# Kernel optimization log

Measured on AMD Instinct MI355X. Metric: run time of the kernel, lower is better.

## Reference

```python
import jax, jax.numpy as jnp
import numpy as np

N_NODES = 50000
N_GRAPHS = 256
IN_DIM = 128
HID = 128
N_LAYERS = 3
N_EDGES = 800000


def setup_inputs() -> dict:
    key = jax.random.key(0)
    ks = jax.random.split(key, 16)
    x = jax.random.normal(ks[0], (N_NODES, IN_DIM), dtype=jnp.float32)
    edge_index = jax.random.randint(ks[1], (2, N_EDGES), 0, N_NODES, dtype=jnp.int64)
    batch = jnp.sort(jax.random.randint(ks[2], (N_NODES,), 0, N_GRAPHS, dtype=jnp.int64))
    inp = {"x": x, "edge_index": edge_index, "batch": batch}
    # SAGEConv params per PyG: lin_l (bias) applied to mean-aggregated neighbors,
    # lin_r (no bias) applied to the root node feature.
    dims = [(IN_DIM, HID)] + [(HID, HID)] * (N_LAYERS - 1)
    for i, (din, dout) in enumerate(dims):
        s = 1.0 / np.sqrt(din)
        inp[f"Wl{i}"] = jax.random.uniform(ks[3 + 3 * i], (din, dout), jnp.float32, -s, s)
        inp[f"bl{i}"] = jax.random.uniform(ks[4 + 3 * i], (dout,), jnp.float32, -s, s)
        inp[f"Wr{i}"] = jax.random.uniform(ks[5 + 3 * i], (din, dout), jnp.float32, -s, s)
    return inp


def _sage_conv(x, src, dst, Wl, bl, Wr):
    # mean aggregation of source-node messages into destination nodes
    msg = x[src]                                               # [E, d] gather
    agg = jax.ops.segment_sum(msg, dst, num_segments=N_NODES)  # [N, d] scatter-add
    deg = jax.ops.segment_sum(jnp.ones((src.shape[0], 1), x.dtype), dst,
                              num_segments=N_NODES)
    agg = agg / jnp.maximum(deg, 1.0)
    return agg @ Wl + bl + x @ Wr


def reference(x, edge_index, batch, Wl0, bl0, Wr0, Wl1, bl1, Wr1, Wl2, bl2, Wr2):
    src, dst = edge_index[0], edge_index[1]
    params = [(Wl0, bl0, Wr0), (Wl1, bl1, Wr1), (Wl2, bl2, Wr2)]
    h = x
    for Wl, bl, Wr in params:
        h = jax.nn.relu(_sage_conv(h, src, dst, Wl, bl, Wr))
        # dropout is a no-op in eval mode
    # meanmax readout over graph ids
    cnt = jax.ops.segment_sum(jnp.ones((h.shape[0], 1), h.dtype), batch,
                              num_segments=N_GRAPHS)
    g_mean = jax.ops.segment_sum(h, batch, num_segments=N_GRAPHS) / jnp.maximum(cnt, 1.0)
    g_max = jax.ops.segment_max(h, batch, num_segments=N_GRAPHS)
    g_max = jnp.where(jnp.isfinite(g_max), g_max, 0.0)  # empty graphs -> 0
    return jnp.concatenate([g_mean, g_max], axis=-1)    # [G, 2*HID]
```

## Files before the change

kernel.cpp:

```cpp
#include <hip/hip_runtime.h>
#include <hip/hip_bf16.h>
#include <stdint.h>

#define N_NODES  50000
#define N_GRAPHS 256
#define DIM      128
#define N_EDGES  800000
#define K2       256
#define N_STRIPS (N_NODES / 16)
#define PAD_CAP  64
#define RO_ROWS  32

typedef __attribute__((ext_vector_type(8))) short  short8;
typedef __attribute__((ext_vector_type(4))) float  floatx4;
typedef __attribute__((ext_vector_type(4))) int    intx4;

__device__ __forceinline__ ushort f2bf(float f) {
    union { float f; uint32_t u; } c; c.f = f;
    uint32_t u = c.u;
    return (ushort)((u + 0x7fffu + ((u >> 16) & 1u)) >> 16);
}
__device__ __forceinline__ float bf2f(ushort b) {
    union { uint32_t u; float f; } c; c.u = ((uint32_t)b) << 16;
    return c.f;
}

#define MB_CONV 6250
#define MB_PREPW (MB_CONV + 384)
#define MB_GB   (MB_PREPW + 196)
#define MB_CNT  (MB_GB + 196)
#define MB_OUT  (MB_CNT + 256)
__global__ __launch_bounds__(256) void k_misc(const float* __restrict__ x, ushort* __restrict__ xb,
                                              const float* __restrict__ Wl0, const float* __restrict__ Wr0,
                                              const float* __restrict__ Wl1, const float* __restrict__ Wr1,
                                              const float* __restrict__ Wl2, const float* __restrict__ Wr2,
                                              ushort* __restrict__ Wt,
                                              const int* __restrict__ batch,
                                              int* __restrict__ gstart, int* __restrict__ gend,
                                              int* __restrict__ cnt, float* __restrict__ out) {
    int b = blockIdx.x, t = threadIdx.x;
    if (b < MB_CONV) {
        int i = b * 256 + t;
        float4 v = ((const float4*)x)[i];
        uint32_t lo = (uint32_t)f2bf(v.x) | ((uint32_t)f2bf(v.y) << 16);
        uint32_t hi = (uint32_t)f2bf(v.z) | ((uint32_t)f2bf(v.w) << 16);
        ((uint2*)xb)[i] = make_uint2(lo, hi);
    } else if (b < MB_PREPW) {
        int i = (b - MB_CONV) * 256 + t;
        int layer = i / (DIM * K2);
        int j = i % (DIM * K2);
        int n = j / K2, k = j % K2;
        const float* Wl = (layer == 0) ? Wl0 : (layer == 1) ? Wl1 : Wl2;
        const float* Wr = (layer == 0) ? Wr0 : (layer == 1) ? Wr1 : Wr2;
        float v = (k < DIM) ? Wl[k * DIM + n] : Wr[(k - DIM) * DIM + n];
        Wt[i] = f2bf(v);
    } else if (b < MB_GB) {
        int i = (b - MB_PREPW) * 256 + t;
        if (i < N_NODES) {
            int g = batch[i];
            if (i == 0) gstart[g] = 0;
            int gn = (i + 1 < N_NODES) ? batch[i + 1] : -1;
            if (gn != g) {
                gend[g] = i + 1;
                if (gn >= 0) gstart[gn] = i + 1;
            }
        }
    } else if (b < MB_CNT) {
        int i = (b - MB_GB) * 256 + t;
        if (i < N_NODES) cnt[i] = 0;
    } else {
        int i = (b - MB_CNT) * 256 + t;
        if (i < N_GRAPHS * 2 * DIM) out[i] = 0.f;
    }
}

__global__ __launch_bounds__(256) void k_build_direct(const int* __restrict__ src,
                                                      const int* __restrict__ dst,
                                                      int* __restrict__ cnt,
                                                      int* __restrict__ padded) {
    int i = blockIdx.x * 256 + threadIdx.x;
    if (i < N_EDGES) {
        int d = dst[i], s = src[i];
        int p = atomicAdd(&cnt[d], 1);
        if (p < PAD_CAP) padded[(size_t)d * PAD_CAP + p] = s;
    }
}

__global__ __launch_bounds__(256) void k_sort_adj(int* __restrict__ padded,
                                                  const int* __restrict__ cnt) {
    int wid  = threadIdx.x >> 6;
    int lane = threadIdx.x & 63;
    int node = blockIdx.x * 4 + wid;
    if (node >= N_NODES) return;
    int deg = cnt[node];
    int m   = deg < PAD_CAP ? deg : PAD_CAP;
    int* lst = padded + (size_t)node * PAD_CAP;
    int v = (lane < m) ? lst[lane] : 0x7fffffff;
    #pragma unroll
    for (int k = 2; k <= 64; k <<= 1) {
        #pragma unroll
        for (int j = k >> 1; j > 0; j >>= 1) {
            int other  = __shfl_xor(v, j, 64);
            bool down  = (lane & k) != 0;
            bool lower = (lane & j) == 0;
            v = (lower ^ down) ? min(v, other) : max(v, other);
        }
    }
    if (lane < m) lst[lane] = v;
}

template <bool OUT_F32>
__global__ __launch_bounds__(256) void k_layer(const ushort* __restrict__ h_in,
                                               const int* __restrict__ padded,
                                               const int* __restrict__ cnt,
                                               const ushort* __restrict__ Wt,
                                               const float* __restrict__ bias,
                                               ushort* __restrict__ out_bf,
                                               float* __restrict__ out_f) {
    __shared__ ushort sAgg[16 * DIM];
    __shared__ int    sIdx[16 * PAD_CAP];
    __shared__ int    sCnt[16];
    __shared__ int    sChl[4][17];
    __shared__ int    sNch[4];

    int t    = threadIdx.x;
    int wid  = t >> 6;
    int lane = t & 63;
    int r0   = blockIdx.x * 16;
    const uint32_t* hw = (const uint32_t*)h_in;

    ((intx4*)sIdx)[t] = __builtin_nontemporal_load(
        ((const intx4*)(padded + (size_t)r0 * PAD_CAP)) + t);
    if (t < 16) sCnt[t] = cnt[r0 + t];
    __syncthreads();

    if (lane == 0) {
        int n = 0;
        #pragma unroll
        for (int q = 0; q < 4; ++q) {
            int m = min(sCnt[wid * 4 + q], PAD_CAP);
            for (int e0 = 0; e0 < m; e0 += 16)
                sChl[wid][n++] = q | (e0 << 8);
        }
        sNch[wid] = n;
    }
    #pragma unroll
    for (int q = 0; q < 4; ++q) {
        int node = wid * 4 + q;
        if (sCnt[node] == 0) ((uint32_t*)(sAgg + node * DIM))[lane] = 0u;
    }
    int nch = sNch[wid];

    float ax[4] = {0.f, 0.f, 0.f, 0.f};
    float ay[4] = {0.f, 0.f, 0.f, 0.f};
    uint32_t va[16], vb[16];

    auto issue = [&](int ci, uint32_t (&v)[16]) {
        int ch   = sChl[wid][ci];
        int q    = ch & 255, e0 = ch >> 8;
        int node = wid * 4 + q;
        int m    = min(sCnt[node], PAD_CAP);
        const int* lst = sIdx + node * PAD_CAP;
        #pragma unroll
        for (int k = 0; k < 16; ++k) {
            int ek = e0 + k;
            int id = lst[ek < m ? ek : m - 1];
            v[k] = hw[(size_t)id * 64 + lane];
        }
    };
    auto consume = [&](int ci, uint32_t (&v)[16], bool isLast) {
        int ch   = sChl[wid][ci];
        int q    = ch & 255, e0 = ch >> 8;
        int node = wid * 4 + q;
        int deg  = sCnt[node];
        int m    = min(deg, PAD_CAP);
        #pragma unroll
        for (int k = 0; k < 16; ++k) {
            uint32_t w = (e0 + k < m) ? v[k] : 0u;
            ax[k & 3] += __uint_as_float(w << 16);
            ay[k & 3] += __uint_as_float(w & 0xffff0000u);
        }
        bool lastOfNode = isLast || ((sChl[wid][ci + 1] & 255) != q);
        if (lastOfNode) {
            float axs = (ax[0] + ax[1]) + (ax[2] + ax[3]);
            float ays = (ay[0] + ay[1]) + (ay[2] + ay[3]);
            float inv = 1.0f / (float)(deg > 0 ? deg : 1);
            uint32_t o = (uint32_t)f2bf(axs * inv) | ((uint32_t)f2bf(ays * inv) << 16);
            ((uint32_t*)(sAgg + node * DIM))[lane] = o;
            #pragma unroll
            for (int j = 0; j < 4; ++j) { ax[j] = 0.f; ay[j] = 0.f; }
        }
    };

    if (nch > 0) {
        issue(0, va);
        int i = 0;
        while (true) {
            bool hasB = (i + 1) < nch;
            if (hasB) issue(i + 1, vb);
            consume(i, va, !hasB);
            if (!hasB) break;
            bool hasA = (i + 2) < nch;
            if (hasA) issue(i + 2, va);
            consume(i + 1, vb, !hasA);
            if (!hasA) break;
            i += 2;
        }
    }
    __syncthreads();

    int row  = lane & 15;
    int quad = lane >> 4;
    short8 a[8];
    const ushort* srow = sAgg + row * DIM + quad * 8;
    #pragma unroll
    for (int ks = 0; ks < 4; ++ks) a[ks] = *(const short8*)(srow + ks * 32);
    const ushort* hrow = h_in + (size_t)(r0 + row) * DIM + quad * 8;
    #pragma unroll
    for (int ks = 0; ks < 4; ++ks) a[4 + ks] = *(const short8*)(hrow + ks * 32);

    #pragma unroll
    for (int c = 0; c < 2; ++c) {
        int ct  = wid * 2 + c;
        int col = ct * 16 + row;
        const ushort* wrow = Wt + (size_t)col * K2 + quad * 8;
        floatx4 acc = {0.f, 0.f, 0.f, 0.f};
        #pragma unroll
        for (int ks = 0; ks < 8; ++ks) {
            short8 b = *(const short8*)(wrow + ks * 32);
            acc = __builtin_amdgcn_mfma_f32_16x16x32_bf16(a[ks], b, acc, 0, 0, 0);
        }
        float bv = bias[col];
        #pragma unroll
        for (int r = 0; r < 4; ++r) {
            int m = r0 + quad * 4 + r;
            float v = acc[r] + bv;
            v = v > 0.f ? v : 0.f;
            if (OUT_F32) __builtin_nontemporal_store(v, &out_f[(size_t)m * DIM + col]);
            else         __builtin_nontemporal_store(f2bf(v), &out_bf[(size_t)m * DIM + col]);
        }
    }
}

__global__ __launch_bounds__(128) void k_readout(const float* __restrict__ h,
                                                 const int* __restrict__ batch,
                                                 float* __restrict__ out) {
    int d  = threadIdx.x;
    int n0 = blockIdx.x * RO_ROWS;
    int n1 = min(n0 + RO_ROWS, N_NODES);
    int cur = -1; float sum = 0.f, mx = 0.f;
    for (int i = n0; i < n1; ++i) {
        int g = batch[i];
        if (g != cur) {
            if (cur >= 0) {
                atomicAdd(&out[cur * 2 * DIM + d], sum);
                atomicMax((int*)&out[cur * 2 * DIM + DIM + d], __float_as_int(mx));
            }
            cur = g; sum = 0.f; mx = 0.f;
        }
        float v = __builtin_nontemporal_load(&h[(size_t)i * DIM + d]);
        sum += v; mx = fmaxf(mx, v);
    }
    if (cur >= 0) {
        atomicAdd(&out[cur * 2 * DIM + d], sum);
        atomicMax((int*)&out[cur * 2 * DIM + DIM + d], __float_as_int(mx));
    }
}

__global__ __launch_bounds__(256) void k_finalize(float* __restrict__ out,
                                                  const int* __restrict__ gstart,
                                                  const int* __restrict__ gend) {
    int i = blockIdx.x * 256 + threadIdx.x;
    if (i < N_GRAPHS * DIM) {
        int g = i / DIM, d = i % DIM;
        int c = gend[g] - gstart[g];
        out[g * 2 * DIM + d] /= (float)(c > 0 ? c : 1);
    }
}

extern "C" void kernel_launch(void* const* d_in, const int* in_sizes, int n_in,
                              void* d_out, int out_size, void* d_ws, size_t ws_size,
                              hipStream_t stream) {
    const float* x     = (const float*)d_in[0];
    const int*   ei    = (const int*)d_in[1];
    const int*   src   = ei;
    const int*   dst   = ei + N_EDGES;
    const int*   batch = (const int*)d_in[2];
    const float* Wl[3] = {(const float*)d_in[3], (const float*)d_in[6], (const float*)d_in[9]};
    const float* bl[3] = {(const float*)d_in[4], (const float*)d_in[7], (const float*)d_in[10]};
    const float* Wr[3] = {(const float*)d_in[5], (const float*)d_in[8], (const float*)d_in[11]};
    float* out = (float*)d_out;

    char* base = (char*)d_ws;
    size_t o = 0;
    auto alloc = [&](size_t b) -> char* {
        char* p = base + o;
        o = (o + b + 255) & ~(size_t)255;
        return p;
    };
    int*     gstart = (int*)alloc((size_t)N_GRAPHS * 4);
    int*     gend   = (int*)alloc((size_t)N_GRAPHS * 4);
    int*     cnt    = (int*)alloc((size_t)N_NODES * 4);
    int*     padded = (int*)alloc((size_t)N_NODES * PAD_CAP * 4);
    ushort*  xb     = (ushort*)alloc((size_t)N_NODES * DIM * 2);
    ushort*  ha     = (ushort*)alloc((size_t)N_NODES * DIM * 2);
    ushort*  hb     = (ushort*)alloc((size_t)N_NODES * DIM * 2);
    float*   h3     = (float*)alloc((size_t)N_NODES * DIM * 4);
    ushort*  Wt     = (ushort*)alloc((size_t)3 * DIM * K2 * 2);
    (void)ws_size; (void)n_in; (void)in_sizes; (void)out_size;

    k_misc<<<MB_OUT, 256, 0, stream>>>(x, xb, Wl[0], Wr[0], Wl[1], Wr[1], Wl[2], Wr[2],
                                       Wt, batch, gstart, gend, cnt, out);
    k_build_direct<<<(N_EDGES + 255) / 256, 256, 0, stream>>>(src, dst, cnt, padded);
    k_sort_adj<<<(N_NODES + 3) / 4, 256, 0, stream>>>(padded, cnt);

    k_layer<false><<<N_STRIPS, 256, 0, stream>>>(xb, padded, cnt, Wt,                bl[0], ha, nullptr);
    k_layer<false><<<N_STRIPS, 256, 0, stream>>>(ha, padded, cnt, Wt + DIM * K2,     bl[1], hb, nullptr);
    k_layer<true ><<<N_STRIPS, 256, 0, stream>>>(hb, padded, cnt, Wt + 2 * DIM * K2, bl[2], nullptr, h3);

    k_readout<<<(N_NODES + RO_ROWS - 1) / RO_ROWS, 128, 0, stream>>>(h3, batch, out);
    k_finalize<<<(N_GRAPHS * DIM + 255) / 256, 256, 0, stream>>>(out, gstart, gend);
}
```

Before: 349.4 us.

## Fuse adjacency sort into first layer and readout into last layer

The separate per-node bitonic sort of the padded adjacency lists moves into layer 0, which sorts each node's list in shared memory and writes it back for later layers. The readout is fused into layer 2: the fp32 output tile stays in shared memory and is reduced per graph with atomic add and max, so the fp32 h3 buffer and its write and reread go away. This removes two kernel launches and about 25 MB of global traffic. In exchange layer 0 does extra shuffle work, and the readout now issues more atomics per 16-row strip than the old 32-row blocks did.

After: 327.4 us. -6.3%, faster.

```diff
diff --git a/kernel.cpp b/kernel.cpp
--- a/kernel.cpp
+++ b/kernel.cpp
@@ -9,7 +9,6 @@
 #define K2       256
 #define N_STRIPS (N_NODES / 16)
 #define PAD_CAP  64
-#define RO_ROWS  32
 
 typedef __attribute__((ext_vector_type(8))) short  short8;
 typedef __attribute__((ext_vector_type(4))) float  floatx4;
@@ -19,10 +18,6 @@
     union { float f; uint32_t u; } c; c.f = f;
     uint32_t u = c.u;
     return (ushort)((u + 0x7fffu + ((u >> 16) & 1u)) >> 16);
-}
-__device__ __forceinline__ float bf2f(ushort b) {
-    union { uint32_t u; float f; } c; c.u = ((uint32_t)b) << 16;
-    return c.f;
 }
 
 #define MB_CONV 6250
@@ -86,42 +81,22 @@
     }
 }
 
-__global__ __launch_bounds__(256) void k_sort_adj(int* __restrict__ padded,
-                                                  const int* __restrict__ cnt) {
-    int wid  = threadIdx.x >> 6;
-    int lane = threadIdx.x & 63;
-    int node = blockIdx.x * 4 + wid;
-    if (node >= N_NODES) return;
-    int deg = cnt[node];
-    int m   = deg < PAD_CAP ? deg : PAD_CAP;
-    int* lst = padded + (size_t)node * PAD_CAP;
-    int v = (lane < m) ? lst[lane] : 0x7fffffff;
-    #pragma unroll
-    for (int k = 2; k <= 64; k <<= 1) {
-        #pragma unroll
-        for (int j = k >> 1; j > 0; j >>= 1) {
-            int other  = __shfl_xor(v, j, 64);
-            bool down  = (lane & k) != 0;
-            bool lower = (lane & j) == 0;
-            v = (lower ^ down) ? min(v, other) : max(v, other);
-        }
-    }
-    if (lane < m) lst[lane] = v;
-}
-
-template <bool OUT_F32>
+template <int MODE>
 __global__ __launch_bounds__(256) void k_layer(const ushort* __restrict__ h_in,
-                                               const int* __restrict__ padded,
+                                               int* __restrict__ padded,
                                                const int* __restrict__ cnt,
                                                const ushort* __restrict__ Wt,
                                                const float* __restrict__ bias,
                                                ushort* __restrict__ out_bf,
-                                               float* __restrict__ out_f) {
+                                               const int* __restrict__ batch,
+                                               float* __restrict__ gout) {
     __shared__ ushort sAgg[16 * DIM];
     __shared__ int    sIdx[16 * PAD_CAP];
     __shared__ int    sCnt[16];
     __shared__ int    sChl[4][17];
     __shared__ int    sNch[4];
+    __shared__ int    sGb[(MODE == 2) ? 16 : 1];
+    __shared__ float  hTile[(MODE == 2) ? 16 * DIM : 1];
 
     int t    = threadIdx.x;
     int wid  = t >> 6;
@@ -132,7 +107,33 @@
     ((intx4*)sIdx)[t] = __builtin_nontemporal_load(
         ((const intx4*)(padded + (size_t)r0 * PAD_CAP)) + t);
     if (t < 16) sCnt[t] = cnt[r0 + t];
+    if (MODE == 2 && t >= 16 && t < 32) sGb[t - 16] = batch[r0 + t - 16];
     __syncthreads();
+
+    if (MODE == 0) {
+        #pragma unroll
+        for (int q = 0; q < 4; ++q) {
+            int nl  = wid * 4 + q;
+            int m   = min(sCnt[nl], PAD_CAP);
+            int* lst = sIdx + nl * PAD_CAP;
+            int v = (lane < m) ? lst[lane] : 0x7fffffff;
+            #pragma unroll
+            for (int k = 2; k <= 64; k <<= 1) {
+                #pragma unroll
+                for (int j = k >> 1; j > 0; j >>= 1) {
+                    int other  = __shfl_xor(v, j, 64);
+                    bool down  = (lane & k) != 0;
+                    bool lower = (lane & j) == 0;
+                    v = (lower ^ down) ? min(v, other) : max(v, other);
+                }
+            }
+            if (lane < m) {
+                lst[lane] = v;
+                __builtin_nontemporal_store(v,
+                    &padded[(size_t)(r0 + nl) * PAD_CAP + lane]);
+            }
+        }
+    }
 
     if (lane == 0) {
         int n = 0;
@@ -236,34 +237,30 @@
             int m = r0 + quad * 4 + r;
             float v = acc[r] + bv;
             v = v > 0.f ? v : 0.f;
-            if (OUT_F32) __builtin_nontemporal_store(v, &out_f[(size_t)m * DIM + col]);
-            else         __builtin_nontemporal_store(f2bf(v), &out_bf[(size_t)m * DIM + col]);
-        }
-    }
-}
-
-__global__ __launch_bounds__(128) void k_readout(const float* __restrict__ h,
-                                                 const int* __restrict__ batch,
-                                                 float* __restrict__ out) {
-    int d  = threadIdx.x;
-    int n0 = blockIdx.x * RO_ROWS;
-    int n1 = min(n0 + RO_ROWS, N_NODES);
-    int cur = -1; float sum = 0.f, mx = 0.f;
-    for (int i = n0; i < n1; ++i) {
-        int g = batch[i];
-        if (g != cur) {
-            if (cur >= 0) {
-                atomicAdd(&out[cur * 2 * DIM + d], sum);
-                atomicMax((int*)&out[cur * 2 * DIM + DIM + d], __float_as_int(mx));
+            if (MODE < 2) __builtin_nontemporal_store(f2bf(v), &out_bf[(size_t)m * DIM + col]);
+            else          hTile[(quad * 4 + r) * DIM + col] = v;
+        }
+    }
+
+    if (MODE == 2) {
+        __syncthreads();
+        int d     = t & 127;
+        bool doMax = t >= 128;
+        float s = 0.f, mx = 0.f;
+        int cur = sGb[0];
+        #pragma unroll
+        for (int m = 0; m < 16; ++m) {
+            int g = sGb[m];
+            if (g != cur) {
+                if (doMax) atomicMax((int*)&gout[cur * 2 * DIM + DIM + d], __float_as_int(mx));
+                else       atomicAdd(&gout[cur * 2 * DIM + d], s);
+                cur = g; s = 0.f; mx = 0.f;
             }
-            cur = g; sum = 0.f; mx = 0.f;
-        }
-        float v = __builtin_nontemporal_load(&h[(size_t)i * DIM + d]);
-        sum += v; mx = fmaxf(mx, v);
-    }
-    if (cur >= 0) {
-        atomicAdd(&out[cur * 2 * DIM + d], sum);
-        atomicMax((int*)&out[cur * 2 * DIM + DIM + d], __float_as_int(mx));
+            float v = hTile[m * DIM + d];
+            s += v; mx = fmaxf(mx, v);
+        }
+        if (doMax) atomicMax((int*)&gout[cur * 2 * DIM + DIM + d], __float_as_int(mx));
+        else       atomicAdd(&gout[cur * 2 * DIM + d], s);
     }
 }
 
@@ -305,19 +302,16 @@
     ushort*  xb     = (ushort*)alloc((size_t)N_NODES * DIM * 2);
     ushort*  ha     = (ushort*)alloc((size_t)N_NODES * DIM * 2);
     ushort*  hb     = (ushort*)alloc((size_t)N_NODES * DIM * 2);
-    float*   h3     = (float*)alloc((size_t)N_NODES * DIM * 4);
     ushort*  Wt     = (ushort*)alloc((size_t)3 * DIM * K2 * 2);
     (void)ws_size; (void)n_in; (void)in_sizes; (void)out_size;
 
     k_misc<<<MB_OUT, 256, 0, stream>>>(x, xb, Wl[0], Wr[0], Wl[1], Wr[1], Wl[2], Wr[2],
                                        Wt, batch, gstart, gend, cnt, out);
     k_build_direct<<<(N_EDGES + 255) / 256, 256, 0, stream>>>(src, dst, cnt, padded);
-    k_sort_adj<<<(N_NODES + 3) / 4, 256, 0, stream>>>(padded, cnt);
-
-    k_layer<false><<<N_STRIPS, 256, 0, stream>>>(xb, padded, cnt, Wt,                bl[0], ha, nullptr);
-    k_layer<false><<<N_STRIPS, 256, 0, stream>>>(ha, padded, cnt, Wt + DIM * K2,     bl[1], hb, nullptr);
-    k_layer<true ><<<N_STRIPS, 256, 0, stream>>>(hb, padded, cnt, Wt + 2 * DIM * K2, bl[2], nullptr, h3);
-
-    k_readout<<<(N_NODES + RO_ROWS - 1) / RO_ROWS, 128, 0, stream>>>(h3, batch, out);
+
+    k_layer<0><<<N_STRIPS, 256, 0, stream>>>(xb, padded, cnt, Wt,                bl[0], ha, batch, out);
+    k_layer<1><<<N_STRIPS, 256, 0, stream>>>(ha, padded, cnt, Wt + DIM * K2,     bl[1], hb, batch, out);
+    k_layer<2><<<N_STRIPS, 256, 0, stream>>>(hb, padded, cnt, Wt + 2 * DIM * K2, bl[2], nullptr, batch, out);
+
     k_finalize<<<(N_GRAPHS * DIM + 255) / 256, 256, 0, stream>>>(out, gstart, gend);
 }
```
